# Performance work log

Hardware: AMD Instinct MI355X
Metric: run time of the kernel (lower is better)

Reference implementation:

```python
import jax, jax.numpy as jnp
import numpy as np

B = 4096
OBS_DIM = 1024
E_OUT = 512
H1 = 2048
H2 = 2048


def setup_inputs() -> dict:
    key = jax.random.key(0)
    ks = jax.random.split(key, 12)
    def kaiming(k, shape, fan_in):
        return jax.random.normal(k, shape, dtype=jnp.float32) * np.float32(np.sqrt(2.0 / fan_in))
    obs = jax.random.normal(ks[0], (B, OBS_DIM), dtype=jnp.float32)
    # lineare: Linear(obs_dim, e_outputs), torch weight shape [out, in]
    We = kaiming(ks[1], (E_OUT, OBS_DIM), OBS_DIM)
    be = jax.random.normal(ks[2], (E_OUT,), dtype=jnp.float32) * 0.01
    # obs_dim attention heads, each Linear(e_outputs, 2), stacked
    attn_W = kaiming(ks[3], (OBS_DIM, E_OUT, 2), E_OUT)
    attn_b = jax.random.normal(ks[4], (OBS_DIM, 2), dtype=jnp.float32) * 0.01
    # v_net: Linear(obs_dim,H1)+tanh, Linear(H1,H2)+[dropout(eval:no-op)]+tanh, Linear(H2,1)
    W1 = kaiming(ks[5], (H1, OBS_DIM), OBS_DIM)
    b1 = jnp.zeros((H1,), dtype=jnp.float32)
    W2 = kaiming(ks[6], (H2, H1), H1)
    b2 = jnp.zeros((H2,), dtype=jnp.float32)
    W3 = kaiming(ks[7], (1, H2), H2)
    b3 = jnp.zeros((1,), dtype=jnp.float32)
    return {"obs": obs, "We": We, "be": be, "attn_W": attn_W, "attn_b": attn_b,
            "W1": W1, "b1": b1, "W2": W2, "b2": b2, "W3": W3, "b3": b3}


def reference(obs, We, be, attn_W, attn_b, W1, b1, W2, b2, W3, b3):
    # e = tanh(lineare(obs)) : [B, E_OUT]
    e = jnp.tanh(obs @ We.T + be)
    # all obs_dim attention heads batched into one contraction: [B, OBS_DIM, 2]
    logits = jnp.einsum('be,oec->boc', e, attn_W) + attn_b
    # softmax over the 2 logits, keep prob of class 1 -> Attention [B, OBS_DIM]
    attention = jax.nn.softmax(logits, axis=-1)[..., 1]
    state_attention = obs * attention
    # v_net (eval mode: dropout is identity)
    h = jnp.tanh(state_attention @ W1.T + b1)
    h = jnp.tanh(h @ W2.T + b2)
    v = jnp.squeeze(h @ W3.T + b3, -1)  # [B]
    return (v, attention)
```

## Files before the change

kernel.cpp:

```cpp
#include <hip/hip_runtime.h>
#include <hip/hip_bf16.h>

typedef unsigned short u16;
typedef u16 u16x4 __attribute__((ext_vector_type(4)));
typedef u16 u16x8 __attribute__((ext_vector_type(8)));
typedef __bf16 bf16x8 __attribute__((ext_vector_type(8)));
typedef float f32x4 __attribute__((ext_vector_type(4)));

__device__ __forceinline__ u16 f2bf(float f) {
  unsigned u = __float_as_uint(f);
  u += 0x7FFFu + ((u >> 16) & 1u);
  return (u16)(u >> 16);
}
__device__ __forceinline__ float bf2f(u16 h) {
  return __uint_as_float(((unsigned)h) << 16);
}
__device__ __forceinline__ float tanh_fast(float x) {
  float t = __expf(2.0f * x);
  return 1.0f - 2.0f / (t + 1.0f);
}
__device__ __forceinline__ float sigmoid_fast(float x) {
  return 1.0f / (1.0f + __expf(-x));
}

__device__ __forceinline__ void cvt4(const float* __restrict__ s, u16* __restrict__ d, int q) {
  float4 v = ((const float4*)s)[q];
  u16x4 o = { f2bf(v.x), f2bf(v.y), f2bf(v.z), f2bf(v.w) };
  ((u16x4*)d)[q] = o;
}

__global__ __launch_bounds__(256)
void prep_kernel(const float* __restrict__ obs, const float* __restrict__ We,
                 const float* __restrict__ W1, const float* __restrict__ W2,
                 const float* __restrict__ aW, const float* __restrict__ ab,
                 u16* __restrict__ obs_b, u16* __restrict__ We_b,
                 u16* __restrict__ W1_b, u16* __restrict__ W2_b,
                 u16* __restrict__ Wd, float* __restrict__ bd) {
  int q = blockIdx.x * 256 + threadIdx.x;
  if (q < 1048576) { cvt4(obs, obs_b, q); return; }
  q -= 1048576;
  if (q < 131072) { cvt4(We, We_b, q); return; }
  q -= 131072;
  if (q < 524288) { cvt4(W1, W1_b, q); return; }
  q -= 524288;
  if (q < 1048576) { cvt4(W2, W2_b, q); return; }
  q -= 1048576;
  if (q < 131072) {
    int i0 = q * 4;
    int o = i0 >> 9, e0 = i0 & 511;
    const float* p = aW + (size_t)o * 1024 + e0 * 2;
    float4 v0 = *(const float4*)p;
    float4 v1 = *(const float4*)(p + 4);
    u16x4 od = { f2bf(v0.y - v0.x), f2bf(v0.w - v0.z),
                 f2bf(v1.y - v1.x), f2bf(v1.w - v1.z) };
    *(u16x4*)(Wd + i0) = od;
    if (q < 256) {
      float4 a0 = *(const float4*)(ab + q * 8);
      float4 a1 = *(const float4*)(ab + q * 8 + 4);
      float4 ob = { a0.y - a0.x, a0.w - a0.z, a1.y - a1.x, a1.w - a1.z };
      *(float4*)(bd + q * 4) = ob;
    }
  }
}

template <int EP>
__global__ __launch_bounds__(256)
void gemm_bt(const u16* __restrict__ A, const u16* __restrict__ Bt,
             int M, int N, int K,
             const float* __restrict__ bias,
             u16* __restrict__ outb,
             float* __restrict__ outf,
             const float* __restrict__ obs,
             u16* __restrict__ sa) {
  __shared__ __align__(16) u16 As[128 * 32];
  __shared__ __align__(16) u16 Bs[128 * 32];

  const int tid = threadIdx.x;
  const int lane = tid & 63;
  const int wave = tid >> 6;
  const int bm = blockIdx.x;
  const int bn = blockIdx.y;

  const int r0 = tid >> 2;
  const int c0 = (tid & 3) * 8;
  const u16* gA = A + (size_t)(bm * 128 + r0) * K + c0;
  const u16* gB = Bt + (size_t)(bn * 128 + r0) * K + c0;
  const size_t rowStep = (size_t)64 * K;

  u16* wA0 = As + r0 * 32 + c0;
  u16* wA1 = As + (r0 + 64) * 32 + c0;
  u16* wB0 = Bs + r0 * 32 + c0;
  u16* wB1 = Bs + (r0 + 64) * 32 + c0;

  const int wm = (wave >> 1) * 64;
  const int wn = (wave & 1) * 64;
  const int fr = lane & 15;
  const int koff = (lane >> 4) * 8;

  u16x8 pa0 = *(const u16x8*)gA;
  u16x8 pa1 = *(const u16x8*)(gA + rowStep);
  u16x8 pb0 = *(const u16x8*)gB;
  u16x8 pb1 = *(const u16x8*)(gB + rowStep);

  f32x4 acc[4][4];
#pragma unroll
  for (int i = 0; i < 4; ++i)
#pragma unroll
    for (int j = 0; j < 4; ++j)
      acc[i][j] = (f32x4){0.f, 0.f, 0.f, 0.f};

  for (int k0 = 0; k0 < K; k0 += 32) {
    __syncthreads();
    *(u16x8*)wA0 = pa0;
    *(u16x8*)wA1 = pa1;
    *(u16x8*)wB0 = pb0;
    *(u16x8*)wB1 = pb1;
    __syncthreads();

    if (k0 + 32 < K) {
      gA += 32; gB += 32;
      pa0 = *(const u16x8*)gA;
      pa1 = *(const u16x8*)(gA + rowStep);
      pb0 = *(const u16x8*)gB;
      pb1 = *(const u16x8*)(gB + rowStep);
    }

    bf16x8 a[4], b[4];
#pragma unroll
    for (int i = 0; i < 4; ++i)
      a[i] = *(const bf16x8*)(As + (wm + i * 16 + fr) * 32 + koff);
#pragma unroll
    for (int j = 0; j < 4; ++j)
      b[j] = *(const bf16x8*)(Bs + (wn + j * 16 + fr) * 32 + koff);
#pragma unroll
    for (int i = 0; i < 4; ++i)
#pragma unroll
      for (int j = 0; j < 4; ++j)
        acc[i][j] = __builtin_amdgcn_mfma_f32_16x16x32_bf16(a[i], b[j], acc[i][j], 0, 0, 0);
  }

#pragma unroll
  for (int j = 0; j < 4; ++j) {
    const int col = bn * 128 + wn + j * 16 + fr;
    const float bv = bias[col];
#pragma unroll
    for (int i = 0; i < 4; ++i) {
#pragma unroll
      for (int r = 0; r < 4; ++r) {
        const int row = bm * 128 + wm + i * 16 + (lane >> 4) * 4 + r;
        const float x = acc[i][j][r] + bv;
        const size_t idx = (size_t)row * N + col;
        if (EP == 0) {
          outb[idx] = f2bf(tanh_fast(x));
        } else {
          const float att = sigmoid_fast(x);
          outf[idx] = att;
          sa[idx] = f2bf(obs[idx] * att);
        }
      }
    }
  }
}

__global__ __launch_bounds__(256)
void gemv_v(const u16* __restrict__ h2, const float* __restrict__ W3,
            const float* __restrict__ b3, float* __restrict__ out) {
  int g = blockIdx.x * 256 + threadIdx.x;
  int row = g >> 6;
  int lane = g & 63;
  const u16* rp = h2 + (size_t)row * 2048;
  float sum = 0.f;
#pragma unroll
  for (int p = 0; p < 4; ++p) {
    int base = p * 512 + lane * 8;
    u16x8 hv = *(const u16x8*)(rp + base);
    float4 w0 = *(const float4*)(W3 + base);
    float4 w1 = *(const float4*)(W3 + base + 4);
    sum += bf2f(hv[0]) * w0.x + bf2f(hv[1]) * w0.y + bf2f(hv[2]) * w0.z + bf2f(hv[3]) * w0.w;
    sum += bf2f(hv[4]) * w1.x + bf2f(hv[5]) * w1.y + bf2f(hv[6]) * w1.z + bf2f(hv[7]) * w1.w;
  }
#pragma unroll
  for (int off = 32; off > 0; off >>= 1) sum += __shfl_down(sum, off);
  if (lane == 0) out[row] = sum + b3[0];
}

extern "C" void kernel_launch(void* const* d_in, const int* in_sizes, int n_in,
                              void* d_out, int out_size, void* d_ws, size_t ws_size,
                              hipStream_t stream) {
  const float* obs   = (const float*)d_in[0];
  const float* We    = (const float*)d_in[1];
  const float* be    = (const float*)d_in[2];
  const float* attnW = (const float*)d_in[3];
  const float* attnb = (const float*)d_in[4];
  const float* W1    = (const float*)d_in[5];
  const float* b1    = (const float*)d_in[6];
  const float* W2    = (const float*)d_in[7];
  const float* b2    = (const float*)d_in[8];
  const float* W3    = (const float*)d_in[9];
  const float* b3    = (const float*)d_in[10];
  float* out = (float*)d_out;

  char* ws = (char*)d_ws;
  u16*   We_b  = (u16*)(ws + 0x00000000);
  u16*   Wd_b  = (u16*)(ws + 0x00100000);
  u16*   W1_b  = (u16*)(ws + 0x00200000);
  u16*   W2_b  = (u16*)(ws + 0x00600000);
  float* bd    = (float*)(ws + 0x00E00000);
  u16*   obs_b = (u16*)(ws + 0x00E01000);
  u16*   e_b   = (u16*)(ws + 0x01601000);
  u16*   sa_b  = (u16*)(ws + 0x01A01000);
  u16*   h1_b  = (u16*)(ws + 0x02201000);
  u16*   h2_b  = (u16*)(ws + 0x03201000);

  prep_kernel<<<11264, 256, 0, stream>>>(obs, We, W1, W2, attnW, attnb,
                                         obs_b, We_b, W1_b, W2_b, Wd_b, bd);

  gemm_bt<0><<<dim3(32, 4), 256, 0, stream>>>(obs_b, We_b, 4096, 512, 1024, be, e_b, nullptr, nullptr, nullptr);
  gemm_bt<1><<<dim3(32, 8), 256, 0, stream>>>(e_b, Wd_b, 4096, 1024, 512, bd, nullptr, out + 4096, obs, sa_b);
  gemm_bt<0><<<dim3(32, 16), 256, 0, stream>>>(sa_b, W1_b, 4096, 2048, 1024, b1, h1_b, nullptr, nullptr, nullptr);
  gemm_bt<0><<<dim3(32, 16), 256, 0, stream>>>(h1_b, W2_b, 4096, 2048, 2048, b2, h2_b, nullptr, nullptr, nullptr);
  gemv_v<<<1024, 256, 0, stream>>>(h2_b, W3, b3, out);
}
```

Measured before the change: 221.8 us.

## Double-buffer GEMM tiles via async global-to-LDS loads and shrink tile sizes

```diff
diff --git a/kernel.cpp b/kernel.cpp
--- a/kernel.cpp
+++ b/kernel.cpp
@@ -21,6 +21,13 @@
 }
 __device__ __forceinline__ float sigmoid_fast(float x) {
   return 1.0f / (1.0f + __expf(-x));
+}
+
+__device__ __forceinline__ void async16(const void* g, void* lds) {
+  __builtin_amdgcn_global_load_lds(
+      (const __attribute__((address_space(1))) unsigned int*)g,
+      (__attribute__((address_space(3))) unsigned int*)lds,
+      16, 0, 0);
 }
 
 __device__ __forceinline__ void cvt4(const float* __restrict__ s, u16* __restrict__ d, int q) {
@@ -63,7 +70,7 @@
   }
 }
 
-template <int EP>
+template <int BM, int BN, int EP>
 __global__ __launch_bounds__(256)
 void gemm_bt(const u16* __restrict__ A, const u16* __restrict__ Bt,
              int M, int N, int K,
@@ -72,8 +79,14 @@
              float* __restrict__ outf,
              const float* __restrict__ obs,
              u16* __restrict__ sa) {
-  __shared__ __align__(16) u16 As[128 * 32];
-  __shared__ __align__(16) u16 Bs[128 * 32];
+  constexpr int MI = BM / 32;
+  constexpr int NJ = BN / 32;
+  constexpr int CA = BM / 16;
+  constexpr int CHUNKS = (BM + BN) / 16;
+  constexpr int CPW = CHUNKS / 4;
+
+  __shared__ __align__(16) u16 As[2][BM * 32];
+  __shared__ __align__(16) u16 Bs[2][BN * 32];
 
   const int tid = threadIdx.x;
   const int lane = tid & 63;
@@ -81,73 +94,79 @@
   const int bm = blockIdx.x;
   const int bn = blockIdx.y;
 
-  const int r0 = tid >> 2;
-  const int c0 = (tid & 3) * 8;
-  const u16* gA = A + (size_t)(bm * 128 + r0) * K + c0;
-  const u16* gB = Bt + (size_t)(bn * 128 + r0) * K + c0;
-  const size_t rowStep = (size_t)64 * K;
-
-  u16* wA0 = As + r0 * 32 + c0;
-  u16* wA1 = As + (r0 + 64) * 32 + c0;
-  u16* wB0 = Bs + r0 * 32 + c0;
-  u16* wB1 = Bs + (r0 + 64) * 32 + c0;
-
-  const int wm = (wave >> 1) * 64;
-  const int wn = (wave & 1) * 64;
+  const u16* gsrc[CPW];
+  u16* ld0[CPW];
+  u16* ld1[CPW];
+#pragma unroll
+  for (int q = 0; q < CPW; ++q) {
+    const int c = wave * CPW + q;
+    if (c < CA) {
+      const int r = c * 16;
+      gsrc[q] = A + (size_t)(bm * BM + r + (lane >> 2)) * K + (lane & 3) * 8;
+      ld0[q] = &As[0][r * 32];
+      ld1[q] = &As[1][r * 32];
+    } else {
+      const int r = (c - CA) * 16;
+      gsrc[q] = Bt + (size_t)(bn * BN + r + (lane >> 2)) * K + (lane & 3) * 8;
+      ld0[q] = &Bs[0][r * 32];
+      ld1[q] = &Bs[1][r * 32];
+    }
+  }
+
+  const int wm = (wave >> 1) * (BM / 2);
+  const int wn = (wave & 1) * (BN / 2);
   const int fr = lane & 15;
   const int koff = (lane >> 4) * 8;
 
-  u16x8 pa0 = *(const u16x8*)gA;
-  u16x8 pa1 = *(const u16x8*)(gA + rowStep);
-  u16x8 pb0 = *(const u16x8*)gB;
-  u16x8 pb1 = *(const u16x8*)(gB + rowStep);
-
-  f32x4 acc[4][4];
-#pragma unroll
-  for (int i = 0; i < 4; ++i)
-#pragma unroll
-    for (int j = 0; j < 4; ++j)
+  const int T = K >> 5;
+
+#pragma unroll
+  for (int q = 0; q < CPW; ++q) async16(gsrc[q], ld0[q]);
+#pragma unroll
+  for (int q = 0; q < CPW; ++q) gsrc[q] += 32;
+
+  f32x4 acc[MI][NJ];
+#pragma unroll
+  for (int i = 0; i < MI; ++i)
+#pragma unroll
+    for (int j = 0; j < NJ; ++j)
       acc[i][j] = (f32x4){0.f, 0.f, 0.f, 0.f};
 
-  for (int k0 = 0; k0 < K; k0 += 32) {
+  for (int k = 0; k < T; ++k) {
     __syncthreads();
-    *(u16x8*)wA0 = pa0;
-    *(u16x8*)wA1 = pa1;
-    *(u16x8*)wB0 = pb0;
-    *(u16x8*)wB1 = pb1;
-    __syncthreads();
-
-    if (k0 + 32 < K) {
-      gA += 32; gB += 32;
-      pa0 = *(const u16x8*)gA;
-      pa1 = *(const u16x8*)(gA + rowStep);
-      pb0 = *(const u16x8*)gB;
-      pb1 = *(const u16x8*)(gB + rowStep);
-    }
-
-    bf16x8 a[4], b[4];
-#pragma unroll
-    for (int i = 0; i < 4; ++i)
-      a[i] = *(const bf16x8*)(As + (wm + i * 16 + fr) * 32 + koff);
-#pragma unroll
-    for (int j = 0; j < 4; ++j)
-      b[j] = *(const bf16x8*)(Bs + (wn + j * 16 + fr) * 32 + koff);
-#pragma unroll
-    for (int i = 0; i < 4; ++i)
-#pragma unroll
-      for (int j = 0; j < 4; ++j)
+    if (k + 1 < T) {
+      const int nxt = (k + 1) & 1;
+#pragma unroll
+      for (int q = 0; q < CPW; ++q) async16(gsrc[q], nxt ? ld1[q] : ld0[q]);
+#pragma unroll
+      for (int q = 0; q < CPW; ++q) gsrc[q] += 32;
+    }
+    const u16* Ar = &As[k & 1][0];
+    const u16* Br = &Bs[k & 1][0];
+
+    bf16x8 a[MI], b[NJ];
+#pragma unroll
+    for (int i = 0; i < MI; ++i)
+      a[i] = *(const bf16x8*)(Ar + (wm + i * 16 + fr) * 32 + koff);
+#pragma unroll
+    for (int j = 0; j < NJ; ++j)
+      b[j] = *(const bf16x8*)(Br + (wn + j * 16 + fr) * 32 + koff);
+#pragma unroll
+    for (int i = 0; i < MI; ++i)
+#pragma unroll
+      for (int j = 0; j < NJ; ++j)
         acc[i][j] = __builtin_amdgcn_mfma_f32_16x16x32_bf16(a[i], b[j], acc[i][j], 0, 0, 0);
   }
 
 #pragma unroll
-  for (int j = 0; j < 4; ++j) {
-    const int col = bn * 128 + wn + j * 16 + fr;
+  for (int j = 0; j < NJ; ++j) {
+    const int col = bn * BN + wn + j * 16 + fr;
     const float bv = bias[col];
 #pragma unroll
-    for (int i = 0; i < 4; ++i) {
+    for (int i = 0; i < MI; ++i) {
 #pragma unroll
       for (int r = 0; r < 4; ++r) {
-        const int row = bm * 128 + wm + i * 16 + (lane >> 4) * 4 + r;
+        const int row = bm * BM + wm + i * 16 + (lane >> 4) * 4 + r;
         const float x = acc[i][j][r] + bv;
         const size_t idx = (size_t)row * N + col;
         if (EP == 0) {
@@ -215,9 +234,9 @@
   prep_kernel<<<11264, 256, 0, stream>>>(obs, We, W1, W2, attnW, attnb,
                                          obs_b, We_b, W1_b, W2_b, Wd_b, bd);
 
-  gemm_bt<0><<<dim3(32, 4), 256, 0, stream>>>(obs_b, We_b, 4096, 512, 1024, be, e_b, nullptr, nullptr, nullptr);
-  gemm_bt<1><<<dim3(32, 8), 256, 0, stream>>>(e_b, Wd_b, 4096, 1024, 512, bd, nullptr, out + 4096, obs, sa_b);
-  gemm_bt<0><<<dim3(32, 16), 256, 0, stream>>>(sa_b, W1_b, 4096, 2048, 1024, b1, h1_b, nullptr, nullptr, nullptr);
-  gemm_bt<0><<<dim3(32, 16), 256, 0, stream>>>(h1_b, W2_b, 4096, 2048, 2048, b2, h2_b, nullptr, nullptr, nullptr);
+  gemm_bt<64, 64, 0><<<dim3(64, 8), 256, 0, stream>>>(obs_b, We_b, 4096, 512, 1024, be, e_b, nullptr, nullptr, nullptr);
+  gemm_bt<64, 64, 1><<<dim3(64, 16), 256, 0, stream>>>(e_b, Wd_b, 4096, 1024, 512, bd, nullptr, out + 4096, obs, sa_b);
+  gemm_bt<128, 64, 0><<<dim3(32, 32), 256, 0, stream>>>(sa_b, W1_b, 4096, 2048, 1024, b1, h1_b, nullptr, nullptr, nullptr);
+  gemm_bt<128, 64, 0><<<dim3(32, 32), 256, 0, stream>>>(h1_b, W2_b, 4096, 2048, 2048, b2, h2_b, nullptr, nullptr, nullptr);
   gemv_v<<<1024, 256, 0, stream>>>(h2_b, W3, b3, out);
 }
```

Result: no change. 218.5 us (-1.5%).
